# Kernel optimization log

Measured on AMD Instinct MI355X. Metric: run time of the kernel, lower is better.

The kernel has to match this reference:

```python
import jax, jax.numpy as jnp
import numpy as np

B, S, D, F, E, TOP_K = 4, 1024, 512, 2048, 16, 2
TEMPERATURE = 0.5
STD = 0.02


def setup_inputs() -> dict:
    key = jax.random.key(0)
    ks = jax.random.split(key, 9)
    f32 = jnp.float32
    return {
        "x": jax.random.normal(ks[0], (B, S, D), f32),
        # router gate: Linear(D, D//2) -> ReLU -> Linear(D//2, E)
        "gate_w1": jax.random.normal(ks[1], (D, D // 2), f32) * STD,
        "gate_b1": jnp.zeros((D // 2,), f32),
        "gate_w2": jax.random.normal(ks[2], (D // 2, E), f32) * STD,
        "gate_b2": jnp.zeros((E,), f32),
        # stacked expert weights (E experts, each D->F->D)
        "up_w": jax.random.normal(ks[3], (E, D, F), f32) * STD,
        "up_b": jnp.zeros((E, F), f32),
        "down_w": jax.random.normal(ks[4], (E, F, D), f32) * STD,
        "down_b": jnp.zeros((E, D), f32),
    }


def reference(x, gate_w1, gate_b1, gate_w2, gate_b2, up_w, up_b, down_w, down_b):
    num_experts = up_w.shape[0]
    # ---- router ----
    h = jax.nn.relu(x @ gate_w1 + gate_b1)                      # [B,S,D//2]
    scores = h @ gate_w2 + gate_b2                              # [B,S,E]
    routing_probs = jax.nn.softmax(scores / TEMPERATURE, axis=-1)
    # load-balance loss: MSE(mean usage, uniform)
    batch_usage = routing_probs.mean(axis=(0, 1))               # [E]
    load_balance_loss = jnp.mean((batch_usage - 1.0 / num_experts) ** 2)
    # ---- top-k routing weights, renormalized via softmax over selected scores ----
    top_vals, top_idx = jax.lax.top_k(routing_probs, TOP_K)     # [B,S,K]
    top_probs = jax.nn.softmax(top_vals, axis=-1)               # [B,S,K]
    # scatter per-token top-k probs into dense [B,S,E] combine weights
    expert_probs = jnp.einsum(
        "bske,bsk->bse", jax.nn.one_hot(top_idx, num_experts, dtype=x.dtype), top_probs
    )
    # ---- every expert computed densely on all tokens, masked combine (faithful to source) ----
    hid = jax.nn.gelu(
        jnp.einsum("bsd,edf->ebsf", x, up_w) + up_b[:, None, None, :],
        approximate=False,
    )                                                            # [E,B,S,F]
    expert_out = jnp.einsum("ebsf,efd->ebsd", hid, down_w) + down_b[:, None, None, :]
    output = jnp.einsum("ebsd,bse->bsd", expert_out, expert_probs)  # [B,S,D]
    return output, load_balance_loss, routing_probs
```

## Files before the change

### kernel.cpp

```cpp
#include <hip/hip_runtime.h>
#include <hip/hip_bf16.h>

#define NTOK 4096
#define DIM  512
#define DH   256
#define NE   16
#define FF   2048
#define CAP  8192
#define MAXTILES 80
#define TEMP_INV 2.0f

#define OUT_LOSS  (NTOK * DIM)
#define OUT_PROBS (NTOK * DIM + 1)

#define WS_CNT    0
#define WS_USAGE  64
#define WS_NTILES 128
#define WS_DESC   256
#define WS_WTS    1024
#define WS_LISTS  36864
#define WS_H      (1ull<<20)
#define WS_G      (1ull<<20)
#define WS_TUP    (16ull<<20)
#define WS_PAIR   (16ull<<20)
#define WS_TDN    (48ull<<20)
#define WS_HID    (80ull<<20)

typedef __attribute__((ext_vector_type(8))) short bf16x8;
typedef __attribute__((ext_vector_type(8))) unsigned short u16x8;
typedef __attribute__((ext_vector_type(4))) float f32x4;

__device__ __forceinline__ unsigned short f2bf(float f) {
  union { float f; unsigned u; } c; c.f = f;
  return (unsigned short)((c.u + 0x7FFFu + ((c.u >> 16) & 1u)) >> 16);
}

#define GLOAD16(gp, lp) __builtin_amdgcn_global_load_lds( \
    (const __attribute__((address_space(1))) void*)(gp), \
    (__attribute__((address_space(3))) void*)(lp), 16, 0, 0)

__launch_bounds__(256)
__global__ void fused0_kernel(const float* __restrict__ x,
                              const float* __restrict__ w1,
                              const float* __restrict__ b1,
                              const float* __restrict__ up_w,
                              const float* __restrict__ down_w,
                              float* __restrict__ H,
                              unsigned short* __restrict__ Tup,
                              unsigned short* __restrict__ Tdn) {
  __shared__ __align__(16) char smem[33792];
  int bx = blockIdx.x, tid = threadIdx.x;

  if (bx < 512) {
    float* As = (float*)smem;
    float* Bs = (float*)(smem + 32 * 68 * 4);
    int mb = bx >> 3, nb = bx & 7;
    int tok0 = mb * 64, n0 = nb * 32;
    int ty = tid >> 4, tx = tid & 15;
    float acc[4][2];
#pragma unroll
    for (int i = 0; i < 4; ++i) { acc[i][0] = 0.f; acc[i][1] = 0.f; }

    for (int kc = 0; kc < 16; ++kc) {
      int k0 = kc * 32;
      {
        int tk = tid >> 2, kg = (tid & 3) * 8;
        const float* xp = x + (size_t)(tok0 + tk) * DIM + k0 + kg;
        float4 v0 = *(const float4*)xp;
        float4 v1 = *(const float4*)(xp + 4);
        As[(kg + 0) * 68 + tk] = v0.x; As[(kg + 1) * 68 + tk] = v0.y;
        As[(kg + 2) * 68 + tk] = v0.z; As[(kg + 3) * 68 + tk] = v0.w;
        As[(kg + 4) * 68 + tk] = v1.x; As[(kg + 5) * 68 + tk] = v1.y;
        As[(kg + 6) * 68 + tk] = v1.z; As[(kg + 7) * 68 + tk] = v1.w;
      }
      {
        int k = tid >> 3, nn = (tid & 7) * 4;
        *(float4*)&Bs[k * 36 + nn] = *(const float4*)(w1 + (size_t)(k0 + k) * DH + n0 + nn);
      }
      __syncthreads();
#pragma unroll 8
      for (int k = 0; k < 32; ++k) {
        float4 a = *(const float4*)&As[k * 68 + ty * 4];
        float2 b = *(const float2*)&Bs[k * 36 + tx * 2];
#pragma unroll
        for (int i = 0; i < 4; ++i) {
          float av = (i == 0) ? a.x : (i == 1) ? a.y : (i == 2) ? a.z : a.w;
          acc[i][0] = fmaf(av, b.x, acc[i][0]);
          acc[i][1] = fmaf(av, b.y, acc[i][1]);
        }
      }
      __syncthreads();
    }
    float bj0 = b1[n0 + tx * 2], bj1 = b1[n0 + tx * 2 + 1];
#pragma unroll
    for (int i = 0; i < 4; ++i) {
      float2 st;
      st.x = fmaxf(acc[i][0] + bj0, 0.f);
      st.y = fmaxf(acc[i][1] + bj1, 0.f);
      *(float2*)(H + (size_t)(tok0 + ty * 4 + i) * DH + n0 + tx * 2) = st;
    }
  } else {
    const float* src; unsigned short* dst; int srcStride;
    if (bx < 1536) {
      int u = bx - 512;
      int e = u >> 6, kc = (u >> 3) & 7, fb = u & 7;
      src = up_w + (size_t)e * DIM * FF + (size_t)kc * 64 * FF + fb * 256;
      srcStride = FF;
      dst = Tup + ((size_t)(e * 8 + kc) * FF + fb * 256) * 64;
    } else {
      int d = bx - 1536;
      int e = d >> 6, kc = (d >> 1) & 31, nb = d & 1;
      src = down_w + (size_t)e * FF * DIM + (size_t)kc * 64 * DIM + nb * 256;
      srcStride = DIM;
      dst = Tdn + ((size_t)(e * 32 + kc) * DIM + nb * 256) * 64;
    }
    unsigned short* L = (unsigned short*)smem;
#pragma unroll
    for (int i = 0; i < 16; ++i) {
      int idx = tid + i * 256;
      int row = idx >> 6, c4 = idx & 63;
      float4 v = *(const float4*)(src + (size_t)row * srcStride + c4 * 4);
      unsigned short* p = L + row * 264 + c4 * 4;
      p[0] = f2bf(v.x); p[1] = f2bf(v.y); p[2] = f2bf(v.z); p[3] = f2bf(v.w);
    }
    __syncthreads();
#pragma unroll
    for (int j = 0; j < 8; ++j) {
      u16x8 pk;
#pragma unroll
      for (int k = 0; k < 8; ++k) pk[k] = L[(j * 8 + k) * 264 + tid];
      *(u16x8*)(dst + (size_t)tid * 64 + j * 8) = pk;
    }
  }
}

__launch_bounds__(256)
__global__ void score_kernel(const float* __restrict__ H,
                             const float* __restrict__ w2,
                             const float* __restrict__ b2,
                             float* __restrict__ out,
                             int* __restrict__ cnt,
                             float* __restrict__ usage,
                             float* __restrict__ wts,
                             int* __restrict__ lists) {
  __shared__ __align__(16) float hs[16][260];
  __shared__ __align__(16) float w2t[16][260];
  __shared__ float ps[16][NE];
  __shared__ float us[4][NE];
  int tid = threadIdx.x;
  int tok0 = blockIdx.x * 16;
  {
    int r = tid >> 4, seg = tid & 15;
    const float* hp = H + (size_t)(tok0 + r) * DH + seg * 16;
    *(float4*)&hs[r][seg * 16 + 0]  = *(const float4*)(hp + 0);
    *(float4*)&hs[r][seg * 16 + 4]  = *(const float4*)(hp + 4);
    *(float4*)&hs[r][seg * 16 + 8]  = *(const float4*)(hp + 8);
    *(float4*)&hs[r][seg * 16 + 12] = *(const float4*)(hp + 12);
  }
  {
    float4 a = *(const float4*)(w2 + (size_t)tid * 16 + 0);
    float4 b = *(const float4*)(w2 + (size_t)tid * 16 + 4);
    float4 c = *(const float4*)(w2 + (size_t)tid * 16 + 8);
    float4 d = *(const float4*)(w2 + (size_t)tid * 16 + 12);
    w2t[0][tid] = a.x;  w2t[1][tid] = a.y;  w2t[2][tid] = a.z;  w2t[3][tid] = a.w;
    w2t[4][tid] = b.x;  w2t[5][tid] = b.y;  w2t[6][tid] = b.z;  w2t[7][tid] = b.w;
    w2t[8][tid] = c.x;  w2t[9][tid] = c.y;  w2t[10][tid] = c.z; w2t[11][tid] = c.w;
    w2t[12][tid] = d.x; w2t[13][tid] = d.y; w2t[14][tid] = d.z; w2t[15][tid] = d.w;
  }
  __syncthreads();
  int t = tid >> 4, e = tid & 15;
  float s = b2[e];
#pragma unroll 4
  for (int j4 = 0; j4 < 64; ++j4) {
    float4 hv = *(const float4*)&hs[t][j4 * 4];
    float4 wv = *(const float4*)&w2t[e][j4 * 4];
    s = fmaf(hv.x, wv.x, fmaf(hv.y, wv.y, fmaf(hv.z, wv.z, fmaf(hv.w, wv.w, s))));
  }
  s *= TEMP_INV;
  float m = s;
#pragma unroll
  for (int d = 1; d < 16; d <<= 1) m = fmaxf(m, __shfl_xor(m, d));
  float p = expf(s - m);
  float sum = p;
#pragma unroll
  for (int d = 1; d < 16; d <<= 1) sum += __shfl_xor(sum, d);
  float prob = p / sum;
  out[OUT_PROBS + (size_t)(tok0 + t) * NE + e] = prob;
  ps[t][e] = prob;
  float v = prob;
  v += __shfl_xor(v, 16);
  v += __shfl_xor(v, 32);
  if ((tid & 63) < 16) us[tid >> 6][e] = v;
  __syncthreads();
  if (tid < 16) atomicAdd(&usage[tid], us[0][tid] + us[1][tid] + us[2][tid] + us[3][tid]);

  if (tid < 16) {
    int tt = tid;
    float v1 = -1.f; int i1 = 0;
    for (int ee = 0; ee < NE; ++ee) { float pv = ps[tt][ee]; if (pv > v1) { v1 = pv; i1 = ee; } }
    float v2 = -1.f; int i2 = 0;
    for (int ee = 0; ee < NE; ++ee) { if (ee == i1) continue; float pv = ps[tt][ee]; if (pv > v2) { v2 = pv; i2 = ee; } }
    float mm = fmaxf(v1, v2);
    float e0 = expf(v1 - mm), e1 = expf(v2 - mm);
    float rs = 1.f / (e0 + e1);
    int gt = tok0 + tt;
    wts[2 * gt]     = e0 * rs;
    wts[2 * gt + 1] = e1 * rs;
    int p1 = atomicAdd(&cnt[i1], 1);
    lists[i1 * CAP + p1] = 2 * gt;
    int p2 = atomicAdd(&cnt[i2], 1);
    lists[i2 * CAP + p2] = 2 * gt + 1;
  }
}

__global__ void sched_kernel(const int* __restrict__ cnt,
                             const float* __restrict__ usage,
                             int* __restrict__ ntiles,
                             int2* __restrict__ desc,
                             float* __restrict__ out_loss) {
  int lane = threadIdx.x;
  int e = lane & 15;
  int c = (lane < 16) ? cnt[e] : 0;
  int tl = (c + 127) >> 7;
  int v = tl;
#pragma unroll
  for (int d = 1; d < 16; d <<= 1) {
    int u = __shfl_up(v, d);
    if (lane >= d) v += u;
  }
  int excl = v - tl;
  int tot = __shfl(v, 15);
  if (lane == 0) *ntiles = tot;
  if (lane < 16) {
    for (int i = 0; i < tl; ++i) desc[excl + i] = make_int2(e, i << 7);
    float d0 = usage[e] * (1.f / 4096.f) - (1.f / 16.f);
    float ls = d0 * d0;
#pragma unroll
    for (int d = 1; d < 16; d <<= 1) ls += __shfl_xor(ls, d);
    if (lane == 0) *out_loss = ls * (1.f / 16.f);
  }
}

__launch_bounds__(256)
__global__ void gather_kernel(const float* __restrict__ x,
                              const int* __restrict__ cnt,
                              const int* __restrict__ ntiles,
                              const int2* __restrict__ desc,
                              const int* __restrict__ lists,
                              unsigned short* __restrict__ G) {
  int ty = blockIdx.x;
  if (ty >= *ntiles) return;
  int2 dd = desc[ty];
  int e = dd.x, i0 = dd.y;
  int cntE = cnt[e];
  int tid = threadIdx.x, r = tid >> 1, h = tid & 1;
  int aidx = i0 + r;
  bool valid = aidx < cntE;
  int slot = valid ? lists[e * CAP + aidx] : 0;
  const float* xrow = x + (size_t)(slot >> 1) * DIM;
  unsigned short* gb = G + (size_t)ty * 65536;
#pragma unroll
  for (int c4 = 0; c4 < 4; ++c4) {
    int chunk = h * 4 + c4;
    unsigned short* dst = gb + (size_t)chunk * 8192 + r * 64;
#pragma unroll
    for (int j = 0; j < 8; ++j) {
      u16x8 pk;
      if (valid) {
        float4 u = *(const float4*)(xrow + chunk * 64 + j * 8);
        float4 w = *(const float4*)(xrow + chunk * 64 + j * 8 + 4);
        pk[0] = f2bf(u.x); pk[1] = f2bf(u.y); pk[2] = f2bf(u.z); pk[3] = f2bf(u.w);
        pk[4] = f2bf(w.x); pk[5] = f2bf(w.y); pk[6] = f2bf(w.z); pk[7] = f2bf(w.w);
      } else {
        pk = u16x8{0, 0, 0, 0, 0, 0, 0, 0};
      }
      *(u16x8*)(dst + j * 8) = pk;
    }
  }
}

__launch_bounds__(256)
__global__ void up_kernel(const unsigned short* __restrict__ G,
                          const unsigned short* __restrict__ Tup,
                          const float* __restrict__ up_b,
                          const int* __restrict__ ntiles,
                          const int2* __restrict__ desc,
                          unsigned short* __restrict__ hid) {
  int ty = blockIdx.y;
  if (ty >= *ntiles) return;
  int e = desc[ty].x;
  int f0 = blockIdx.x * 128;
  __shared__ __align__(16) unsigned short Ab[2][128 * 64];
  __shared__ __align__(16) unsigned short Bb[2][128 * 64];
  int tid = threadIdx.x, lane = tid & 63, wid = tid >> 6;
  const unsigned short* Asrc = G + (size_t)ty * 65536;
  const unsigned short* Bsrc = Tup + ((size_t)(e * 8) * FF + f0) * 64;

  int wr = wid >> 1, wc = wid & 1, ln15 = lane & 15, lq = lane >> 4;
  f32x4 acc[4][4];
#pragma unroll
  for (int i = 0; i < 4; ++i)
#pragma unroll
    for (int j = 0; j < 4; ++j) acc[i][j] = f32x4{0.f, 0.f, 0.f, 0.f};

#define UP_STAGE(b, kc) do {                                          \
    const unsigned short* a_ = Asrc + (size_t)(kc) * 8192;            \
    const unsigned short* b_ = Bsrc + (size_t)(kc) * FF * 64;         \
    _Pragma("unroll")                                                 \
    for (int i_ = 0; i_ < 4; ++i_) {                                  \
      int off_ = (wid * 4 + i_) * 512;                                \
      GLOAD16(a_ + off_ + lane * 8, &Ab[b][off_]);                    \
      GLOAD16(b_ + off_ + lane * 8, &Bb[b][off_]);                    \
    }                                                                 \
  } while (0)

  UP_STAGE(0, 0);
  asm volatile("s_waitcnt vmcnt(0)" ::: "memory");
  __syncthreads();
  int cur = 0;
  for (int kc = 0; kc < 8; ++kc) {
    if (kc < 7) UP_STAGE(cur ^ 1, kc + 1);
    const unsigned short* As = Ab[cur];
    const unsigned short* Bs = Bb[cur];
#pragma unroll
    for (int ksub = 0; ksub < 2; ++ksub) {
      bf16x8 a[4], b[4];
      int g = (ksub << 2) + lq;
#pragma unroll
      for (int mi = 0; mi < 4; ++mi)
        a[mi] = *(const bf16x8*)(As + ((wr << 6) + (mi << 4) + ln15) * 64 + (g << 3));
#pragma unroll
      for (int ni = 0; ni < 4; ++ni)
        b[ni] = *(const bf16x8*)(Bs + ((wc << 6) + (ni << 4) + ln15) * 64 + (g << 3));
#pragma unroll
      for (int mi = 0; mi < 4; ++mi)
#pragma unroll
        for (int ni = 0; ni < 4; ++ni)
          acc[mi][ni] = __builtin_amdgcn_mfma_f32_16x16x32_bf16(a[mi], b[ni], acc[mi][ni], 0, 0, 0);
    }
    asm volatile("s_waitcnt vmcnt(0)" ::: "memory");
    __syncthreads();
    cur ^= 1;
  }
#pragma unroll
  for (int mi = 0; mi < 4; ++mi) {
    int row = (wr << 6) + (mi << 4) + (lq << 2);
#pragma unroll
    for (int ni = 0; ni < 4; ++ni) {
      int col = (wc << 6) + (ni << 4) + ln15;
      float bias = up_b[e * FF + f0 + col];
      size_t base = ((size_t)(ty * 32 + (f0 >> 6) + (col >> 6)) * 128 + row) * 64 + (col & 63);
#pragma unroll
      for (int q = 0; q < 4; ++q) {
        float vv = acc[mi][ni][q] + bias;
        float gl = 0.5f * vv * (1.f + erff(vv * 0.70710678118f));
        hid[base + (size_t)q * 64] = f2bf(gl);
      }
    }
  }
#undef UP_STAGE
}

__launch_bounds__(256)
__global__ void down_kernel(const unsigned short* __restrict__ hid,
                            const unsigned short* __restrict__ Tdn,
                            const float* __restrict__ down_b,
                            const int* __restrict__ cnt,
                            const int* __restrict__ ntiles,
                            const int2* __restrict__ desc,
                            const int* __restrict__ lists,
                            float* __restrict__ pairbuf) {
  int ty = blockIdx.y;
  if (ty >= *ntiles) return;
  int2 dd = desc[ty];
  int e = dd.x, i0 = dd.y;
  int cntE = cnt[e];
  int n0 = blockIdx.x * 64;
  __shared__ __align__(16) unsigned short Ab[2][128 * 64];
  __shared__ __align__(16) unsigned short Bb[2][64 * 64];
  int tid = threadIdx.x, lane = tid & 63, wid = tid >> 6;
  const unsigned short* Asrc = hid + (size_t)ty * 32 * 8192;
  const unsigned short* Bsrc = Tdn + ((size_t)(e * 32) * DIM + n0) * 64;

  int wr = wid >> 1, wc = wid & 1, ln15 = lane & 15, lq = lane >> 4;
  f32x4 acc[4][2];
#pragma unroll
  for (int i = 0; i < 4; ++i) { acc[i][0] = f32x4{0.f,0.f,0.f,0.f}; acc[i][1] = f32x4{0.f,0.f,0.f,0.f}; }

#define DN_STAGE(b, kc) do {                                          \
    const unsigned short* a_ = Asrc + (size_t)(kc) * 8192;            \
    const unsigned short* b_ = Bsrc + (size_t)(kc) * DIM * 64;        \
    _Pragma("unroll")                                                 \
    for (int i_ = 0; i_ < 4; ++i_) {                                  \
      int off_ = (wid * 4 + i_) * 512;                                \
      GLOAD16(a_ + off_ + lane * 8, &Ab[b][off_]);                    \
    }                                                                 \
    _Pragma("unroll")                                                 \
    for (int i_ = 0; i_ < 2; ++i_) {                                  \
      int off_ = (wid * 2 + i_) * 512;                                \
      GLOAD16(b_ + off_ + lane * 8, &Bb[b][off_]);                    \
    }                                                                 \
  } while (0)

  DN_STAGE(0, 0);
  asm volatile("s_waitcnt vmcnt(0)" ::: "memory");
  __syncthreads();
  int cur = 0;
  for (int kc = 0; kc < 32; ++kc) {
    if (kc < 31) DN_STAGE(cur ^ 1, kc + 1);
    const unsigned short* As = Ab[cur];
    const unsigned short* Bs = Bb[cur];
#pragma unroll
    for (int ksub = 0; ksub < 2; ++ksub) {
      bf16x8 a[4], b[2];
      int g = (ksub << 2) + lq;
#pragma unroll
      for (int mi = 0; mi < 4; ++mi)
        a[mi] = *(const bf16x8*)(As + ((wr << 6) + (mi << 4) + ln15) * 64 + (g << 3));
#pragma unroll
      for (int ni = 0; ni < 2; ++ni)
        b[ni] = *(const bf16x8*)(Bs + ((wc << 5) + (ni << 4) + ln15) * 64 + (g << 3));
#pragma unroll
      for (int mi = 0; mi < 4; ++mi)
#pragma unroll
        for (int ni = 0; ni < 2; ++ni)
          acc[mi][ni] = __builtin_amdgcn_mfma_f32_16x16x32_bf16(a[mi], b[ni], acc[mi][ni], 0, 0, 0);
    }
    asm volatile("s_waitcnt vmcnt(0)" ::: "memory");
    __syncthreads();
    cur ^= 1;
  }
#pragma unroll
  for (int mi = 0; mi < 4; ++mi) {
    int row = (wr << 6) + (mi << 4) + (lq << 2);
#pragma unroll
    for (int ni = 0; ni < 2; ++ni) {
      int col = n0 + (wc << 5) + (ni << 4) + ln15;
      float bias = down_b[e * DIM + col];
#pragma unroll
      for (int q = 0; q < 4; ++q) {
        int idx = i0 + row + q;
        if (idx < cntE) {
          int slot = lists[e * CAP + idx];
          pairbuf[(size_t)slot * DIM + col] = acc[mi][ni][q] + bias;
        }
      }
    }
  }
#undef DN_STAGE
}

__launch_bounds__(256)
__global__ void combine_kernel(const float* __restrict__ pairbuf,
                               const float* __restrict__ wts,
                               float* __restrict__ out) {
  int t = blockIdx.x;
  int d = threadIdx.x << 1;
  float w0 = wts[2 * t], w1 = wts[2 * t + 1];
  float2 a = *(const float2*)(pairbuf + (size_t)(2 * t) * DIM + d);
  float2 b = *(const float2*)(pairbuf + (size_t)(2 * t + 1) * DIM + d);
  float2 r; r.x = w0 * a.x + w1 * b.x; r.y = w0 * a.y + w1 * b.y;
  *(float2*)(out + (size_t)t * DIM + d) = r;
}

extern "C" void kernel_launch(void* const* d_in, const int* in_sizes, int n_in,
                              void* d_out, int out_size, void* d_ws, size_t ws_size,
                              hipStream_t stream) {
  (void)in_sizes; (void)n_in; (void)out_size; (void)ws_size;
  const float* x   = (const float*)d_in[0];
  const float* gw1 = (const float*)d_in[1];
  const float* gb1 = (const float*)d_in[2];
  const float* gw2 = (const float*)d_in[3];
  const float* gb2 = (const float*)d_in[4];
  const float* uw  = (const float*)d_in[5];
  const float* ub  = (const float*)d_in[6];
  const float* dw  = (const float*)d_in[7];
  const float* db  = (const float*)d_in[8];
  float* out = (float*)d_out;
  char* ws = (char*)d_ws;

  int*   cnt     = (int*)(ws + WS_CNT);
  float* usage   = (float*)(ws + WS_USAGE);
  int*   ntiles  = (int*)(ws + WS_NTILES);
  int2*  desc    = (int2*)(ws + WS_DESC);
  float* wts     = (float*)(ws + WS_WTS);
  int*   lists   = (int*)(ws + WS_LISTS);
  float* H       = (float*)(ws + WS_H);
  unsigned short* G   = (unsigned short*)(ws + WS_G);
  unsigned short* Tup = (unsigned short*)(ws + WS_TUP);
  unsigned short* Tdn = (unsigned short*)(ws + WS_TDN);
  unsigned short* hid = (unsigned short*)(ws + WS_HID);
  float* pairbuf = (float*)(ws + WS_PAIR);

  hipMemsetAsync(d_ws, 0, 1024, stream);
  fused0_kernel<<<2560, 256, 0, stream>>>(x, gw1, gb1, uw, dw, H, Tup, Tdn);
  score_kernel<<<NTOK / 16, 256, 0, stream>>>(H, gw2, gb2, out, cnt, usage, wts, lists);
  sched_kernel<<<1, 64, 0, stream>>>(cnt, usage, ntiles, desc, out + OUT_LOSS);
  gather_kernel<<<MAXTILES, 256, 0, stream>>>(x, cnt, ntiles, desc, lists, G);
  up_kernel<<<dim3(FF / 128, MAXTILES), 256, 0, stream>>>(G, Tup, ub, ntiles, desc, hid);
  down_kernel<<<dim3(DIM / 64, MAXTILES), 256, 0, stream>>>(hid, Tdn, db, cnt, ntiles, desc, lists, pairbuf);
  combine_kernel<<<NTOK, 256, 0, stream>>>(pairbuf, wts, out);
}
```

Baseline: 379.0 us.

## XOR-swizzle bf16 tiles, retile prep kernel, split gather, vectorize combine

Adds an XOR swizzle to the 64-element bf16 rows that are written into Tup, Tdn, G and hid, and to the LDS fragment reads in the up and down MFMA kernels, to avoid LDS bank conflicts. The up kernel now stages its GELU output through LDS so it can write swizzled 16-byte vectors. The prep kernel moves to 64-thread blocks with an 8x4 register tile for the router GEMM and a transpose without LDS for the weight conversion. The gather kernel is split over four y-blocks and combine uses float4. Several unrelated changes land together, and the weight conversion now reads with stride-major scalar loads, which may coalesce less well.

```diff
diff --git a/kernel.cpp b/kernel.cpp
--- a/kernel.cpp
+++ b/kernel.cpp
@@ -39,97 +39,103 @@
     (const __attribute__((address_space(1))) void*)(gp), \
     (__attribute__((address_space(3))) void*)(lp), 16, 0, 0)
 
-__launch_bounds__(256)
-__global__ void fused0_kernel(const float* __restrict__ x,
-                              const float* __restrict__ w1,
-                              const float* __restrict__ b1,
-                              const float* __restrict__ up_w,
-                              const float* __restrict__ down_w,
-                              float* __restrict__ H,
-                              unsigned short* __restrict__ Tup,
-                              unsigned short* __restrict__ Tdn) {
-  __shared__ __align__(16) char smem[33792];
+__launch_bounds__(64)
+__global__ void prep_kernel(const float* __restrict__ x,
+                            const float* __restrict__ w1,
+                            const float* __restrict__ b1,
+                            const float* __restrict__ up_w,
+                            const float* __restrict__ down_w,
+                            float* __restrict__ H,
+                            unsigned short* __restrict__ Tup,
+                            unsigned short* __restrict__ Tdn) {
+  __shared__ __align__(16) float As[32 * 72];
+  __shared__ __align__(16) float Bs[32 * 40];
   int bx = blockIdx.x, tid = threadIdx.x;
 
   if (bx < 512) {
-    float* As = (float*)smem;
-    float* Bs = (float*)(smem + 32 * 68 * 4);
-    int mb = bx >> 3, nb = bx & 7;
-    int tok0 = mb * 64, n0 = nb * 32;
-    int ty = tid >> 4, tx = tid & 15;
-    float acc[4][2];
-#pragma unroll
-    for (int i = 0; i < 4; ++i) { acc[i][0] = 0.f; acc[i][1] = 0.f; }
+    int tok0 = (bx >> 3) * 64, n0 = (bx & 7) * 32;
+    int ty = tid >> 3, tx = tid & 7;
+    float acc[8][4];
+#pragma unroll
+    for (int r = 0; r < 8; ++r)
+#pragma unroll
+      for (int c = 0; c < 4; ++c) acc[r][c] = 0.f;
 
     for (int kc = 0; kc < 16; ++kc) {
       int k0 = kc * 32;
       {
-        int tk = tid >> 2, kg = (tid & 3) * 8;
-        const float* xp = x + (size_t)(tok0 + tk) * DIM + k0 + kg;
-        float4 v0 = *(const float4*)xp;
-        float4 v1 = *(const float4*)(xp + 4);
-        As[(kg + 0) * 68 + tk] = v0.x; As[(kg + 1) * 68 + tk] = v0.y;
-        As[(kg + 2) * 68 + tk] = v0.z; As[(kg + 3) * 68 + tk] = v0.w;
-        As[(kg + 4) * 68 + tk] = v1.x; As[(kg + 5) * 68 + tk] = v1.y;
-        As[(kg + 6) * 68 + tk] = v1.z; As[(kg + 7) * 68 + tk] = v1.w;
+        const float* xp = x + (size_t)(tok0 + tid) * DIM + k0;
+#pragma unroll
+        for (int q = 0; q < 8; ++q) {
+          float4 v = *(const float4*)(xp + q * 4);
+          As[(q * 4 + 0) * 72 + tid] = v.x;
+          As[(q * 4 + 1) * 72 + tid] = v.y;
+          As[(q * 4 + 2) * 72 + tid] = v.z;
+          As[(q * 4 + 3) * 72 + tid] = v.w;
+        }
       }
       {
-        int k = tid >> 3, nn = (tid & 7) * 4;
-        *(float4*)&Bs[k * 36 + nn] = *(const float4*)(w1 + (size_t)(k0 + k) * DH + n0 + nn);
+        int kk = tid >> 1, ns = (tid & 1) * 16;
+#pragma unroll
+        for (int j = 0; j < 4; ++j)
+          *(float4*)&Bs[kk * 40 + ns + j * 4] =
+              *(const float4*)(w1 + (size_t)(k0 + kk) * DH + n0 + ns + j * 4);
       }
       __syncthreads();
 #pragma unroll 8
       for (int k = 0; k < 32; ++k) {
-        float4 a = *(const float4*)&As[k * 68 + ty * 4];
-        float2 b = *(const float2*)&Bs[k * 36 + tx * 2];
-#pragma unroll
-        for (int i = 0; i < 4; ++i) {
-          float av = (i == 0) ? a.x : (i == 1) ? a.y : (i == 2) ? a.z : a.w;
-          acc[i][0] = fmaf(av, b.x, acc[i][0]);
-          acc[i][1] = fmaf(av, b.y, acc[i][1]);
+        float4 a0 = *(const float4*)&As[k * 72 + ty * 8];
+        float4 a1 = *(const float4*)&As[k * 72 + ty * 8 + 4];
+        float4 b  = *(const float4*)&Bs[k * 40 + tx * 4];
+#pragma unroll
+        for (int c = 0; c < 4; ++c) {
+          float bv = (c == 0) ? b.x : (c == 1) ? b.y : (c == 2) ? b.z : b.w;
+          acc[0][c] = fmaf(a0.x, bv, acc[0][c]);
+          acc[1][c] = fmaf(a0.y, bv, acc[1][c]);
+          acc[2][c] = fmaf(a0.z, bv, acc[2][c]);
+          acc[3][c] = fmaf(a0.w, bv, acc[3][c]);
+          acc[4][c] = fmaf(a1.x, bv, acc[4][c]);
+          acc[5][c] = fmaf(a1.y, bv, acc[5][c]);
+          acc[6][c] = fmaf(a1.z, bv, acc[6][c]);
+          acc[7][c] = fmaf(a1.w, bv, acc[7][c]);
         }
       }
       __syncthreads();
     }
-    float bj0 = b1[n0 + tx * 2], bj1 = b1[n0 + tx * 2 + 1];
-#pragma unroll
-    for (int i = 0; i < 4; ++i) {
-      float2 st;
-      st.x = fmaxf(acc[i][0] + bj0, 0.f);
-      st.y = fmaxf(acc[i][1] + bj1, 0.f);
-      *(float2*)(H + (size_t)(tok0 + ty * 4 + i) * DH + n0 + tx * 2) = st;
+    float4 bb = *(const float4*)(b1 + n0 + tx * 4);
+#pragma unroll
+    for (int r = 0; r < 8; ++r) {
+      float4 o;
+      o.x = fmaxf(acc[r][0] + bb.x, 0.f);
+      o.y = fmaxf(acc[r][1] + bb.y, 0.f);
+      o.z = fmaxf(acc[r][2] + bb.z, 0.f);
+      o.w = fmaxf(acc[r][3] + bb.w, 0.f);
+      *(float4*)(H + (size_t)(tok0 + ty * 8 + r) * DH + n0 + tx * 4) = o;
     }
   } else {
-    const float* src; unsigned short* dst; int srcStride;
-    if (bx < 1536) {
-      int u = bx - 512;
-      int e = u >> 6, kc = (u >> 3) & 7, fb = u & 7;
-      src = up_w + (size_t)e * DIM * FF + (size_t)kc * 64 * FF + fb * 256;
-      srcStride = FF;
-      dst = Tup + ((size_t)(e * 8 + kc) * FF + fb * 256) * 64;
+    int cb = bx - 512;
+    const float* src; unsigned short* dst; int stride;
+    if (cb < 4096) {
+      int e = cb >> 8, kc = (cb >> 5) & 7, nb = cb & 31;
+      src = up_w + (size_t)e * DIM * FF + (size_t)kc * 64 * FF + nb * 64;
+      dst = Tup + ((size_t)(e * 8 + kc) * FF + nb * 64) * 64;
+      stride = FF;
     } else {
-      int d = bx - 1536;
-      int e = d >> 6, kc = (d >> 1) & 31, nb = d & 1;
-      src = down_w + (size_t)e * FF * DIM + (size_t)kc * 64 * DIM + nb * 256;
-      srcStride = DIM;
-      dst = Tdn + ((size_t)(e * 32 + kc) * DIM + nb * 256) * 64;
-    }
-    unsigned short* L = (unsigned short*)smem;
-#pragma unroll
-    for (int i = 0; i < 16; ++i) {
-      int idx = tid + i * 256;
-      int row = idx >> 6, c4 = idx & 63;
-      float4 v = *(const float4*)(src + (size_t)row * srcStride + c4 * 4);
-      unsigned short* p = L + row * 264 + c4 * 4;
-      p[0] = f2bf(v.x); p[1] = f2bf(v.y); p[2] = f2bf(v.z); p[3] = f2bf(v.w);
-    }
-    __syncthreads();
-#pragma unroll
-    for (int j = 0; j < 8; ++j) {
+      cb -= 4096;
+      int e = cb >> 8, kc = (cb >> 3) & 31, nb = cb & 7;
+      src = down_w + (size_t)e * FF * DIM + (size_t)kc * 64 * DIM + nb * 64;
+      dst = Tdn + ((size_t)(e * 32 + kc) * DIM + nb * 64) * 64;
+      stride = DIM;
+    }
+    const float* s = src + tid;
+    unsigned short* drow = dst + (size_t)tid * 64;
+    int sx = tid & 7;
+#pragma unroll
+    for (int g = 0; g < 8; ++g) {
       u16x8 pk;
 #pragma unroll
-      for (int k = 0; k < 8; ++k) pk[k] = L[(j * 8 + k) * 264 + tid];
-      *(u16x8*)(dst + (size_t)tid * 64 + j * 8) = pk;
+      for (int j = 0; j < 8; ++j) pk[j] = f2bf(s[(size_t)(g * 8 + j) * stride]);
+      *(u16x8*)(drow + ((g ^ sx) << 3)) = pk;
     }
   }
 }
@@ -258,24 +264,21 @@
   bool valid = aidx < cntE;
   int slot = valid ? lists[e * CAP + aidx] : 0;
   const float* xrow = x + (size_t)(slot >> 1) * DIM;
-  unsigned short* gb = G + (size_t)ty * 65536;
-#pragma unroll
-  for (int c4 = 0; c4 < 4; ++c4) {
-    int chunk = h * 4 + c4;
-    unsigned short* dst = gb + (size_t)chunk * 8192 + r * 64;
-#pragma unroll
-    for (int j = 0; j < 8; ++j) {
-      u16x8 pk;
-      if (valid) {
-        float4 u = *(const float4*)(xrow + chunk * 64 + j * 8);
-        float4 w = *(const float4*)(xrow + chunk * 64 + j * 8 + 4);
-        pk[0] = f2bf(u.x); pk[1] = f2bf(u.y); pk[2] = f2bf(u.z); pk[3] = f2bf(u.w);
-        pk[4] = f2bf(w.x); pk[5] = f2bf(w.y); pk[6] = f2bf(w.z); pk[7] = f2bf(w.w);
-      } else {
-        pk = u16x8{0, 0, 0, 0, 0, 0, 0, 0};
-      }
-      *(u16x8*)(dst + j * 8) = pk;
-    }
+  int chunk = blockIdx.y * 2 + h;
+  unsigned short* dst = G + (size_t)ty * 65536 + (size_t)chunk * 8192 + r * 64;
+  int sx = r & 7;
+#pragma unroll
+  for (int j = 0; j < 8; ++j) {
+    u16x8 pk;
+    if (valid) {
+      float4 u = *(const float4*)(xrow + chunk * 64 + j * 8);
+      float4 w = *(const float4*)(xrow + chunk * 64 + j * 8 + 4);
+      pk[0] = f2bf(u.x); pk[1] = f2bf(u.y); pk[2] = f2bf(u.z); pk[3] = f2bf(u.w);
+      pk[4] = f2bf(w.x); pk[5] = f2bf(w.y); pk[6] = f2bf(w.z); pk[7] = f2bf(w.w);
+    } else {
+      pk = u16x8{0, 0, 0, 0, 0, 0, 0, 0};
+    }
+    *(u16x8*)(dst + ((j ^ sx) << 3)) = pk;
   }
 }
 
@@ -290,8 +293,7 @@
   if (ty >= *ntiles) return;
   int e = desc[ty].x;
   int f0 = blockIdx.x * 128;
-  __shared__ __align__(16) unsigned short Ab[2][128 * 64];
-  __shared__ __align__(16) unsigned short Bb[2][128 * 64];
+  __shared__ __align__(16) unsigned short smem[32768];
   int tid = threadIdx.x, lane = tid & 63, wid = tid >> 6;
   const unsigned short* Asrc = G + (size_t)ty * 65536;
   const unsigned short* Bsrc = Tup + ((size_t)(e * 8) * FF + f0) * 64;
@@ -306,11 +308,13 @@
 #define UP_STAGE(b, kc) do {                                          \
     const unsigned short* a_ = Asrc + (size_t)(kc) * 8192;            \
     const unsigned short* b_ = Bsrc + (size_t)(kc) * FF * 64;         \
+    unsigned short* al_ = smem + (b) * 8192;                          \
+    unsigned short* bl_ = smem + 16384 + (b) * 8192;                  \
     _Pragma("unroll")                                                 \
     for (int i_ = 0; i_ < 4; ++i_) {                                  \
       int off_ = (wid * 4 + i_) * 512;                                \
-      GLOAD16(a_ + off_ + lane * 8, &Ab[b][off_]);                    \
-      GLOAD16(b_ + off_ + lane * 8, &Bb[b][off_]);                    \
+      GLOAD16(a_ + off_ + lane * 8, al_ + off_ + lane * 8);           \
+      GLOAD16(b_ + off_ + lane * 8, bl_ + off_ + lane * 8);           \
     }                                                                 \
   } while (0)
 
@@ -320,18 +324,19 @@
   int cur = 0;
   for (int kc = 0; kc < 8; ++kc) {
     if (kc < 7) UP_STAGE(cur ^ 1, kc + 1);
-    const unsigned short* As = Ab[cur];
-    const unsigned short* Bs = Bb[cur];
+    const unsigned short* As = smem + cur * 8192;
+    const unsigned short* Bs = smem + 16384 + cur * 8192;
 #pragma unroll
     for (int ksub = 0; ksub < 2; ++ksub) {
       bf16x8 a[4], b[4];
       int g = (ksub << 2) + lq;
+      int sw = (g ^ (ln15 & 7)) << 3;
 #pragma unroll
       for (int mi = 0; mi < 4; ++mi)
-        a[mi] = *(const bf16x8*)(As + ((wr << 6) + (mi << 4) + ln15) * 64 + (g << 3));
+        a[mi] = *(const bf16x8*)(As + ((wr << 6) + (mi << 4) + ln15) * 64 + sw);
 #pragma unroll
       for (int ni = 0; ni < 4; ++ni)
-        b[ni] = *(const bf16x8*)(Bs + ((wc << 6) + (ni << 4) + ln15) * 64 + (g << 3));
+        b[ni] = *(const bf16x8*)(Bs + ((wc << 6) + (ni << 4) + ln15) * 64 + sw);
 #pragma unroll
       for (int mi = 0; mi < 4; ++mi)
 #pragma unroll
@@ -342,21 +347,31 @@
     __syncthreads();
     cur ^= 1;
   }
+  unsigned short* Cs = smem;
 #pragma unroll
   for (int mi = 0; mi < 4; ++mi) {
-    int row = (wr << 6) + (mi << 4) + (lq << 2);
 #pragma unroll
     for (int ni = 0; ni < 4; ++ni) {
       int col = (wc << 6) + (ni << 4) + ln15;
       float bias = up_b[e * FF + f0 + col];
-      size_t base = ((size_t)(ty * 32 + (f0 >> 6) + (col >> 6)) * 128 + row) * 64 + (col & 63);
 #pragma unroll
       for (int q = 0; q < 4; ++q) {
+        int row = (wr << 6) + (mi << 4) + (lq << 2) + q;
         float vv = acc[mi][ni][q] + bias;
         float gl = 0.5f * vv * (1.f + erff(vv * 0.70710678118f));
-        hid[base + (size_t)q * 64] = f2bf(gl);
+        Cs[row * 136 + col] = f2bf(gl);
       }
     }
+  }
+  __syncthreads();
+#pragma unroll
+  for (int i = 0; i < 8; ++i) {
+    int seg = tid + i * 256;
+    int row = seg >> 4, c16 = seg & 15;
+    int chunk = ty * 32 + (f0 >> 6) + (c16 >> 3);
+    int slot = (c16 & 7) ^ (row & 7);
+    u16x8 v = *(const u16x8*)(Cs + row * 136 + c16 * 8);
+    *(u16x8*)(hid + ((size_t)chunk * 128 + row) * 64 + (slot << 3)) = v;
   }
 #undef UP_STAGE
 }
@@ -376,8 +391,7 @@
   int e = dd.x, i0 = dd.y;
   int cntE = cnt[e];
   int n0 = blockIdx.x * 64;
-  __shared__ __align__(16) unsigned short Ab[2][128 * 64];
-  __shared__ __align__(16) unsigned short Bb[2][64 * 64];
+  __shared__ __align__(16) unsigned short smem[24576];
   int tid = threadIdx.x, lane = tid & 63, wid = tid >> 6;
   const unsigned short* Asrc = hid + (size_t)ty * 32 * 8192;
   const unsigned short* Bsrc = Tdn + ((size_t)(e * 32) * DIM + n0) * 64;
@@ -390,15 +404,17 @@
 #define DN_STAGE(b, kc) do {                                          \
     const unsigned short* a_ = Asrc + (size_t)(kc) * 8192;            \
     const unsigned short* b_ = Bsrc + (size_t)(kc) * DIM * 64;        \
+    unsigned short* al_ = smem + (b) * 8192;                          \
+    unsigned short* bl_ = smem + 16384 + (b) * 4096;                  \
     _Pragma("unroll")                                                 \
     for (int i_ = 0; i_ < 4; ++i_) {                                  \
       int off_ = (wid * 4 + i_) * 512;                                \
-      GLOAD16(a_ + off_ + lane * 8, &Ab[b][off_]);                    \
+      GLOAD16(a_ + off_ + lane * 8, al_ + off_ + lane * 8);           \
     }                                                                 \
     _Pragma("unroll")                                                 \
     for (int i_ = 0; i_ < 2; ++i_) {                                  \
       int off_ = (wid * 2 + i_) * 512;                                \
-      GLOAD16(b_ + off_ + lane * 8, &Bb[b][off_]);                    \
+      GLOAD16(b_ + off_ + lane * 8, bl_ + off_ + lane * 8);           \
     }                                                                 \
   } while (0)
 
@@ -408,18 +424,19 @@
   int cur = 0;
   for (int kc = 0; kc < 32; ++kc) {
     if (kc < 31) DN_STAGE(cur ^ 1, kc + 1);
-    const unsigned short* As = Ab[cur];
-    const unsigned short* Bs = Bb[cur];
+    const unsigned short* As = smem + cur * 8192;
+    const unsigned short* Bs = smem + 16384 + cur * 4096;
 #pragma unroll
     for (int ksub = 0; ksub < 2; ++ksub) {
       bf16x8 a[4], b[2];
       int g = (ksub << 2) + lq;
+      int sw = (g ^ (ln15 & 7)) << 3;
 #pragma unroll
       for (int mi = 0; mi < 4; ++mi)
-        a[mi] = *(const bf16x8*)(As + ((wr << 6) + (mi << 4) + ln15) * 64 + (g << 3));
+        a[mi] = *(const bf16x8*)(As + ((wr << 6) + (mi << 4) + ln15) * 64 + sw);
 #pragma unroll
       for (int ni = 0; ni < 2; ++ni)
-        b[ni] = *(const bf16x8*)(Bs + ((wc << 5) + (ni << 4) + ln15) * 64 + (g << 3));
+        b[ni] = *(const bf16x8*)(Bs + ((wc << 5) + (ni << 4) + ln15) * 64 + sw);
 #pragma unroll
       for (int mi = 0; mi < 4; ++mi)
 #pragma unroll
@@ -454,13 +471,15 @@
 __global__ void combine_kernel(const float* __restrict__ pairbuf,
                                const float* __restrict__ wts,
                                float* __restrict__ out) {
-  int t = blockIdx.x;
-  int d = threadIdx.x << 1;
+  int idx = blockIdx.x * 256 + threadIdx.x;
+  int t = idx >> 7, d4 = (idx & 127) << 2;
   float w0 = wts[2 * t], w1 = wts[2 * t + 1];
-  float2 a = *(const float2*)(pairbuf + (size_t)(2 * t) * DIM + d);
-  float2 b = *(const float2*)(pairbuf + (size_t)(2 * t + 1) * DIM + d);
-  float2 r; r.x = w0 * a.x + w1 * b.x; r.y = w0 * a.y + w1 * b.y;
-  *(float2*)(out + (size_t)t * DIM + d) = r;
+  float4 a = *(const float4*)(pairbuf + (size_t)(2 * t) * DIM + d4);
+  float4 b = *(const float4*)(pairbuf + (size_t)(2 * t + 1) * DIM + d4);
+  float4 r;
+  r.x = w0 * a.x + w1 * b.x; r.y = w0 * a.y + w1 * b.y;
+  r.z = w0 * a.z + w1 * b.z; r.w = w0 * a.w + w1 * b.w;
+  *(float4*)(out + (size_t)t * DIM + d4) = r;
 }
 
 extern "C" void kernel_launch(void* const* d_in, const int* in_sizes, int n_in,
@@ -493,11 +512,11 @@
   float* pairbuf = (float*)(ws + WS_PAIR);
 
   hipMemsetAsync(d_ws, 0, 1024, stream);
-  fused0_kernel<<<2560, 256, 0, stream>>>(x, gw1, gb1, uw, dw, H, Tup, Tdn);
+  prep_kernel<<<8704, 64, 0, stream>>>(x, gw1, gb1, uw, dw, H, Tup, Tdn);
   score_kernel<<<NTOK / 16, 256, 0, stream>>>(H, gw2, gb2, out, cnt, usage, wts, lists);
   sched_kernel<<<1, 64, 0, stream>>>(cnt, usage, ntiles, desc, out + OUT_LOSS);
-  gather_kernel<<<MAXTILES, 256, 0, stream>>>(x, cnt, ntiles, desc, lists, G);
+  gather_kernel<<<dim3(MAXTILES, 4), 256, 0, stream>>>(x, cnt, ntiles, desc, lists, G);
   up_kernel<<<dim3(FF / 128, MAXTILES), 256, 0, stream>>>(G, Tup, ub, ntiles, desc, hid);
   down_kernel<<<dim3(DIM / 64, MAXTILES), 256, 0, stream>>>(hid, Tdn, db, cnt, ntiles, desc, lists, pairbuf);
-  combine_kernel<<<NTOK, 256, 0, stream>>>(pairbuf, wts, out);
-}
+  combine_kernel<<<NTOK * DIM / 4 / 256, 256, 0, stream>>>(pairbuf, wts, out);
+}
```

Result: faster. 363.8 us (-4.0%).
